# Performance work log

Hardware: AMD Instinct MI355X
Metric: run time of the kernel (lower is better)

## Reference

```python
import jax, jax.numpy as jnp
import numpy as np

DIM = 1024
NHEADS = 16
HEAD_DIM = DIM // NHEADS


def setup_inputs() -> dict:
    key = jax.random.key(0)
    ks = jax.random.split(key, 11)
    B, S = 4, 2048
    scale = 1.0 / np.sqrt(DIM)
    inp = {
        "Q": jax.random.normal(ks[0], (B, S, DIM), jnp.float32),
        "K": jax.random.normal(ks[1], (B, S, DIM), jnp.float32),
        "V": jax.random.normal(ks[2], (B, S, DIM), jnp.float32),
        "Wq": jax.random.normal(ks[3], (DIM, DIM), jnp.float32) * scale,
        "bq": jnp.zeros((DIM,), jnp.float32),
        "Wk": jax.random.normal(ks[4], (DIM, DIM), jnp.float32) * scale,
        "bk": jnp.zeros((DIM,), jnp.float32),
        "Wv": jax.random.normal(ks[5], (DIM, DIM), jnp.float32) * scale,
        "bv": jnp.zeros((DIM,), jnp.float32),
        "Wo": jax.random.normal(ks[6], (DIM, DIM), jnp.float32) * scale,
        "bo": jnp.zeros((DIM,), jnp.float32),
    }
    return inp


def _split_heads(x):
    # [B, S, D] -> [B, H, S, hd]
    B, S, _ = x.shape
    return x.reshape(B, S, NHEADS, HEAD_DIM).transpose(0, 2, 1, 3)


def reference(Q, K, V, Wq, bq, Wk, bk, Wv, bv, Wo, bo):
    q = _split_heads(Q @ Wq + bq)  # [B,H,S,hd]
    k = _split_heads(K @ Wk + bk)
    v = _split_heads(V @ Wv + bv)
    scores = jnp.einsum("bhqd,bhkd->bhqk", q, k) / np.sqrt(HEAD_DIM)
    attn = jax.nn.softmax(scores, axis=-1)  # dropout p=0 -> identity
    out = jnp.einsum("bhqk,bhkd->bhqd", attn, v)  # [B,H,S,hd]
    B, H, S, hd = out.shape
    out = out.transpose(0, 2, 1, 3).reshape(B, S, H * hd)
    return out @ Wo + bo
```

## Files before the change

kernel.cpp:

```cpp
#include <hip/hip_runtime.h>
#include <hip/hip_bf16.h>
#include <math.h>

#define DIM     1024
#define NHEADS  16
#define HD      64
#define BATCH   4
#define SEQ     2048
#define M_TOT   (BATCH * SEQ)
#define QSCALE  0.180336880111f

using short8 = __attribute__((ext_vector_type(8))) short;
using f32x4  = __attribute__((ext_vector_type(4))) float;

__device__ inline unsigned short f2bf(float x) {
    __hip_bfloat16 h = __float2bfloat16(x);
    unsigned short u;
    __builtin_memcpy(&u, &h, sizeof(u));
    return u;
}
__device__ inline void st_o(float* p, float v)          { *p = v; }
__device__ inline void st_o(unsigned short* p, float v) { *p = f2bf(v); }

__device__ inline void async16(const void* g, void* l) {
    __builtin_amdgcn_global_load_lds(
        (const __attribute__((address_space(1))) void*)g,
        (__attribute__((address_space(3))) void*)l, 16, 0, 0);
}

__global__ __launch_bounds__(256) void cvt_bf16(const float* __restrict__ src,
                                                unsigned short* __restrict__ dst) {
    const size_t i = ((size_t)blockIdx.x * 256 + threadIdx.x) * 16;
    unsigned short tmp[16];
    #pragma unroll
    for (int p = 0; p < 4; ++p) {
        const float4 v = *(const float4*)(src + i + p * 4);
        tmp[p * 4 + 0] = f2bf(v.x); tmp[p * 4 + 1] = f2bf(v.y);
        tmp[p * 4 + 2] = f2bf(v.z); tmp[p * 4 + 3] = f2bf(v.w);
    }
    *(short8*)(dst + i)     = *(short8*)&tmp[0];
    *(short8*)(dst + i + 8) = *(short8*)&tmp[8];
}

__global__ __launch_bounds__(256) void wcvt(const float* __restrict__ W,
                                            unsigned short* __restrict__ Wt) {
    __shared__ unsigned short tile[32][33];
    const int t = threadIdx.x;
    const int tx = t & 31, ty = t >> 5;
    const int n0 = blockIdx.x * 32, k0 = blockIdx.y * 32;
    #pragma unroll
    for (int i = 0; i < 4; ++i) {
        const int kk = ty + i * 8;
        tile[kk][tx] = f2bf(W[(size_t)(k0 + kk) * DIM + n0 + tx]);
    }
    __syncthreads();
    #pragma unroll
    for (int i = 0; i < 4; ++i) {
        const int nn = ty + i * 8;
        Wt[(size_t)(n0 + nn) * DIM + k0 + tx] = tile[tx][nn];
    }
}

__global__ __launch_bounds__(256) void vtrans(const unsigned short* __restrict__ vf,
                                              unsigned short* __restrict__ vt) {
    __shared__ unsigned short tile[64][72];
    const int t = threadIdx.x;
    const int b = blockIdx.z, h = blockIdx.y, s0 = blockIdx.x * 64;
    const int r = t >> 2, c = (t & 3) * 16;
    const unsigned short* src = vf + (size_t)(b * SEQ + s0 + r) * DIM + h * HD + c;
    *(short8*)&tile[r][c]     = *(const short8*)src;
    *(short8*)&tile[r][c + 8] = *(const short8*)(src + 8);
    __syncthreads();
    unsigned short tmp[16];
    #pragma unroll
    for (int j = 0; j < 16; ++j) tmp[j] = tile[c + j][r];
    unsigned short* dst = vt + ((size_t)(b * NHEADS + h) * HD + r) * SEQ + s0 + c;
    *(short8*)dst       = *(short8*)&tmp[0];
    *(short8*)(dst + 8) = *(short8*)&tmp[8];
}

template <typename TY>
__global__ __launch_bounds__(256) void gemm_a16(
    const unsigned short* __restrict__ A, const unsigned short* __restrict__ Wt,
    const float* __restrict__ bias, TY* __restrict__ Y, float scale)
{
    __shared__ unsigned short As[128 * 32];
    __shared__ unsigned short Bs[128 * 32];
    const int t = threadIdx.x;
    const int lane = t & 63, wv = t >> 6;
    const int wm = wv >> 1, wn = wv & 1;
    const int l16 = lane & 15, lq = lane >> 4;
    const int m0 = blockIdx.y * 128, n0 = blockIdx.x * 128;
    const int lrow = lane >> 2;
    const int lcol = (lane & 3) * 8;

    f32x4 acc[4][4] = {};

    for (int k0 = 0; k0 < DIM; k0 += 32) {
        #pragma unroll
        for (int c = 0; c < 2; ++c) {
            const int ci  = wv * 2 + c;
            const int row = ci * 16 + lrow;
            async16(A  + (size_t)(m0 + row) * DIM + k0 + lcol, &As[ci * 512]);
            async16(Wt + (size_t)(n0 + row) * DIM + k0 + lcol, &Bs[ci * 512]);
        }
        __syncthreads();

        short8 af[4], bfr[4];
        #pragma unroll
        for (int mi = 0; mi < 4; ++mi)
            af[mi] = *(const short8*)&As[(wm * 64 + mi * 16 + l16) * 32 + lq * 8];
        #pragma unroll
        for (int nj = 0; nj < 4; ++nj)
            bfr[nj] = *(const short8*)&Bs[(wn * 64 + nj * 16 + l16) * 32 + lq * 8];
        #pragma unroll
        for (int mi = 0; mi < 4; ++mi)
            #pragma unroll
            for (int nj = 0; nj < 4; ++nj)
                acc[mi][nj] = __builtin_amdgcn_mfma_f32_16x16x32_bf16(
                    af[mi], bfr[nj], acc[mi][nj], 0, 0, 0);
        __syncthreads();
    }

    #pragma unroll
    for (int mi = 0; mi < 4; ++mi)
        #pragma unroll
        for (int nj = 0; nj < 4; ++nj) {
            const int row = m0 + wm * 64 + mi * 16 + lq * 4;
            const int col = n0 + wn * 64 + nj * 16 + l16;
            const float bb = bias[col];
            #pragma unroll
            for (int r = 0; r < 4; ++r)
                st_o(&Y[(size_t)(row + r) * DIM + col], (acc[mi][nj][r] + bb) * scale);
        }
}

__global__ __launch_bounds__(256) void attn_mfma(
    const unsigned short* qbuf, const unsigned short* __restrict__ kbuf,
    const unsigned short* __restrict__ vtb, unsigned short* ctx)
{
    __shared__ unsigned short Qs[64][72];
    __shared__ unsigned short Ks[64][72];
    __shared__ unsigned short Vs[64][72];
    __shared__ unsigned short Ps[64][72];

    const int t = threadIdx.x;
    const int lane = t & 63, wv = t >> 6;
    const int l16 = lane & 15, lq = lane >> 4;
    const int b = blockIdx.z, h = blockIdx.y;
    const int q0 = blockIdx.x * 64;
    const size_t base  = ((size_t)b * SEQ) * DIM + h * HD;
    const size_t vbase = ((size_t)(b * NHEADS + h)) * HD * SEQ;

    {
        const int r = t >> 2, c = (t & 3) * 16;
        const unsigned short* src = qbuf + base + (size_t)(q0 + r) * DIM + c;
        *(short8*)&Qs[r][c]     = *(const short8*)src;
        *(short8*)&Qs[r][c + 8] = *(const short8*)(src + 8);
    }
    const short8 aq0 = *(const short8*)&Qs[wv * 16 + l16][lq * 8];
    const short8 aq1 = *(const short8*)&Qs[wv * 16 + l16][32 + lq * 8];

    float l_part[4] = {0.f, 0.f, 0.f, 0.f};
    f32x4 O[4] = {};

    for (int s0 = 0; s0 < SEQ; s0 += 64) {
        __syncthreads();
        {
            const int r = t >> 2, c = (t & 3) * 16;
            const unsigned short* src = kbuf + base + (size_t)(s0 + r) * DIM + c;
            *(short8*)&Ks[r][c]     = *(const short8*)src;
            *(short8*)&Ks[r][c + 8] = *(const short8*)(src + 8);
        }
        {
            const int d = t >> 2, c = (t & 3) * 16;
            const unsigned short* src = vtb + vbase + (size_t)d * SEQ + s0 + c;
            *(short8*)&Vs[d][c]     = *(const short8*)src;
            *(short8*)&Vs[d][c + 8] = *(const short8*)(src + 8);
        }
        __syncthreads();

        f32x4 sa[4] = {};
        #pragma unroll
        for (int ti = 0; ti < 4; ++ti) {
            const short8 bk0 = *(const short8*)&Ks[ti * 16 + l16][lq * 8];
            const short8 bk1 = *(const short8*)&Ks[ti * 16 + l16][32 + lq * 8];
            sa[ti] = __builtin_amdgcn_mfma_f32_16x16x32_bf16(aq0, bk0, sa[ti], 0, 0, 0);
            sa[ti] = __builtin_amdgcn_mfma_f32_16x16x32_bf16(aq1, bk1, sa[ti], 0, 0, 0);
        }

        #pragma unroll
        for (int r = 0; r < 4; ++r) {
            const float v0 = __builtin_amdgcn_exp2f(sa[0][r]);
            const float v1 = __builtin_amdgcn_exp2f(sa[1][r]);
            const float v2 = __builtin_amdgcn_exp2f(sa[2][r]);
            const float v3 = __builtin_amdgcn_exp2f(sa[3][r]);
            l_part[r] += (v0 + v1) + (v2 + v3);
            const int prow = wv * 16 + lq * 4 + r;
            Ps[prow][l16]      = f2bf(v0);
            Ps[prow][16 + l16] = f2bf(v1);
            Ps[prow][32 + l16] = f2bf(v2);
            Ps[prow][48 + l16] = f2bf(v3);
        }

        #pragma unroll
        for (int kp = 0; kp < 2; ++kp) {
            const short8 ap = *(const short8*)&Ps[wv * 16 + l16][kp * 32 + lq * 8];
            #pragma unroll
            for (int dt = 0; dt < 4; ++dt) {
                const short8 bv = *(const short8*)&Vs[dt * 16 + l16][kp * 32 + lq * 8];
                O[dt] = __builtin_amdgcn_mfma_f32_16x16x32_bf16(ap, bv, O[dt], 0, 0, 0);
            }
        }
    }

    #pragma unroll
    for (int r = 0; r < 4; ++r) {
        float l = l_part[r];
        #pragma unroll
        for (int msk = 1; msk < 16; msk <<= 1) l += __shfl_xor(l, msk);
        const float inv = 1.0f / l;
        const int orow = wv * 16 + lq * 4 + r;
        #pragma unroll
        for (int dt = 0; dt < 4; ++dt)
            Ps[orow][dt * 16 + l16] = f2bf(O[dt][r] * inv);
    }
    __syncthreads();
    {
        const int r = t >> 2, c = (t & 3) * 16;
        unsigned short* dst = ctx + base + (size_t)(q0 + r) * DIM + c;
        *(short8*)dst       = *(const short8*)&Ps[r][c];
        *(short8*)(dst + 8) = *(const short8*)&Ps[r][c + 8];
    }
}

extern "C" void kernel_launch(void* const* d_in, const int* in_sizes, int n_in,
                              void* d_out, int out_size, void* d_ws, size_t ws_size,
                              hipStream_t stream) {
    const float* Q  = (const float*)d_in[0];
    const float* K  = (const float*)d_in[1];
    const float* V  = (const float*)d_in[2];
    const float* Wq = (const float*)d_in[3];
    const float* bq = (const float*)d_in[4];
    const float* Wk = (const float*)d_in[5];
    const float* bk = (const float*)d_in[6];
    const float* Wv = (const float*)d_in[7];
    const float* bv = (const float*)d_in[8];
    const float* Wo = (const float*)d_in[9];
    const float* bo = (const float*)d_in[10];
    float* out = (float*)d_out;

    const size_t eW = (size_t)DIM * DIM;
    const size_t eB = (size_t)M_TOT * DIM;
    unsigned short* p   = (unsigned short*)d_ws;
    unsigned short* wtq = p; p += eW;
    unsigned short* wtk = p; p += eW;
    unsigned short* wtv = p; p += eW;
    unsigned short* wto = p; p += eW;
    unsigned short* bufA = p; p += eB;
    unsigned short* bufB = p; p += eB;
    unsigned short* bufC = p; p += eB;
    unsigned short* bufD = p; p += eB;
    unsigned short* bufE = p;

    const dim3 gw(32, 32);
    wcvt<<<gw, 256, 0, stream>>>(Wq, wtq);
    wcvt<<<gw, 256, 0, stream>>>(Wk, wtk);
    wcvt<<<gw, 256, 0, stream>>>(Wv, wtv);
    wcvt<<<gw, 256, 0, stream>>>(Wo, wto);

    const int cvt_blocks = (int)(eB / (256 * 16));
    const dim3 gg(DIM / 128, M_TOT / 128);

    cvt_bf16<<<cvt_blocks, 256, 0, stream>>>(V, bufA);
    gemm_a16<unsigned short><<<gg, 256, 0, stream>>>(bufA, wtv, bv, bufC, 1.0f);
    vtrans<<<dim3(SEQ / 64, NHEADS, BATCH), 256, 0, stream>>>(bufC, bufE);

    cvt_bf16<<<cvt_blocks, 256, 0, stream>>>(Q, bufA);
    cvt_bf16<<<cvt_blocks, 256, 0, stream>>>(K, bufB);
    gemm_a16<unsigned short><<<gg, 256, 0, stream>>>(bufA, wtq, bq, bufC, QSCALE);
    gemm_a16<unsigned short><<<gg, 256, 0, stream>>>(bufB, wtk, bk, bufD, 1.0f);

    attn_mfma<<<dim3(SEQ / 64, NHEADS, BATCH), 256, 0, stream>>>(bufC, bufD, bufE, bufC);

    gemm_a16<float><<<gg, 256, 0, stream>>>(bufC, wto, bo, out, 1.0f);
}
```

Baseline: 434.6 us.

## Batch launches, compute V transposed via GEMM, split attention keys across waves

Merges the four weight conversions and the three input conversions into single launches, and fuses the Q and K projections into one grid. It computes V already transposed by swapping GEMM operands with a row bias, which removes the separate transpose kernel. The attention kernel is restructured so each wave handles all 64 queries over its own slice of keys with per-wave LDS and no per-iteration block barriers. Partial outputs and row sums are then reduced across waves through LDS. This cuts launch count and synchronisation, at the cost of more registers per wave and an extra cross-wave reduction at the end.

```diff
diff --git a/kernel.cpp b/kernel.cpp
--- a/kernel.cpp
+++ b/kernel.cpp
@@ -28,22 +28,39 @@
         (__attribute__((address_space(3))) void*)l, 16, 0, 0);
 }
 
-__global__ __launch_bounds__(256) void cvt_bf16(const float* __restrict__ src,
-                                                unsigned short* __restrict__ dst) {
+__global__ __launch_bounds__(256) void cvt3(
+    const float* __restrict__ sq, const float* __restrict__ sk, const float* __restrict__ sv,
+    unsigned short* __restrict__ dq, unsigned short* __restrict__ dk, unsigned short* __restrict__ dv)
+{
+    const float* s; unsigned short* d;
+    if      (blockIdx.y == 0) { s = sq; d = dq; }
+    else if (blockIdx.y == 1) { s = sk; d = dk; }
+    else                      { s = sv; d = dv; }
     const size_t i = ((size_t)blockIdx.x * 256 + threadIdx.x) * 16;
     unsigned short tmp[16];
     #pragma unroll
     for (int p = 0; p < 4; ++p) {
-        const float4 v = *(const float4*)(src + i + p * 4);
-        tmp[p * 4 + 0] = f2bf(v.x); tmp[p * 4 + 1] = f2bf(v.y);
-        tmp[p * 4 + 2] = f2bf(v.z); tmp[p * 4 + 3] = f2bf(v.w);
-    }
-    *(short8*)(dst + i)     = *(short8*)&tmp[0];
-    *(short8*)(dst + i + 8) = *(short8*)&tmp[8];
-}
-
-__global__ __launch_bounds__(256) void wcvt(const float* __restrict__ W,
-                                            unsigned short* __restrict__ Wt) {
+        const float4 v = *(const float4*)(s + i + p * 4);
+        tmp[p*4+0] = f2bf(v.x); tmp[p*4+1] = f2bf(v.y);
+        tmp[p*4+2] = f2bf(v.z); tmp[p*4+3] = f2bf(v.w);
+    }
+    *(short8*)(d + i)     = *(short8*)&tmp[0];
+    *(short8*)(d + i + 8) = *(short8*)&tmp[8];
+}
+
+__global__ __launch_bounds__(256) void wcvt4(
+    const float* __restrict__ w0, const float* __restrict__ w1,
+    const float* __restrict__ w2, const float* __restrict__ w3,
+    unsigned short* __restrict__ o0, unsigned short* __restrict__ o1,
+    unsigned short* __restrict__ o2, unsigned short* __restrict__ o3)
+{
+    const float* W; unsigned short* Wt;
+    switch (blockIdx.z) {
+        case 0:  W = w0; Wt = o0; break;
+        case 1:  W = w1; Wt = o1; break;
+        case 2:  W = w2; Wt = o2; break;
+        default: W = w3; Wt = o3; break;
+    }
     __shared__ unsigned short tile[32][33];
     const int t = threadIdx.x;
     const int tx = t & 31, ty = t >> 5;
@@ -61,28 +78,10 @@
     }
 }
 
-__global__ __launch_bounds__(256) void vtrans(const unsigned short* __restrict__ vf,
-                                              unsigned short* __restrict__ vt) {
-    __shared__ unsigned short tile[64][72];
-    const int t = threadIdx.x;
-    const int b = blockIdx.z, h = blockIdx.y, s0 = blockIdx.x * 64;
-    const int r = t >> 2, c = (t & 3) * 16;
-    const unsigned short* src = vf + (size_t)(b * SEQ + s0 + r) * DIM + h * HD + c;
-    *(short8*)&tile[r][c]     = *(const short8*)src;
-    *(short8*)&tile[r][c + 8] = *(const short8*)(src + 8);
-    __syncthreads();
-    unsigned short tmp[16];
-    #pragma unroll
-    for (int j = 0; j < 16; ++j) tmp[j] = tile[c + j][r];
-    unsigned short* dst = vt + ((size_t)(b * NHEADS + h) * HD + r) * SEQ + s0 + c;
-    *(short8*)dst       = *(short8*)&tmp[0];
-    *(short8*)(dst + 8) = *(short8*)&tmp[8];
-}
-
-template <typename TY>
-__global__ __launch_bounds__(256) void gemm_a16(
-    const unsigned short* __restrict__ A, const unsigned short* __restrict__ Wt,
-    const float* __restrict__ bias, TY* __restrict__ Y, float scale)
+template <bool BROW, typename TY>
+__device__ __forceinline__ void gemm_body(
+    const unsigned short* __restrict__ A, const unsigned short* __restrict__ Bt,
+    const float* __restrict__ bias, TY* __restrict__ Y, int N, float scale)
 {
     __shared__ unsigned short As[128 * 32];
     __shared__ unsigned short Bs[128 * 32];
@@ -91,8 +90,7 @@
     const int wm = wv >> 1, wn = wv & 1;
     const int l16 = lane & 15, lq = lane >> 4;
     const int m0 = blockIdx.y * 128, n0 = blockIdx.x * 128;
-    const int lrow = lane >> 2;
-    const int lcol = (lane & 3) * 8;
+    const int lrow = lane >> 2, lcol = (lane & 3) * 8;
 
     f32x4 acc[4][4] = {};
 
@@ -102,10 +100,9 @@
             const int ci  = wv * 2 + c;
             const int row = ci * 16 + lrow;
             async16(A  + (size_t)(m0 + row) * DIM + k0 + lcol, &As[ci * 512]);
-            async16(Wt + (size_t)(n0 + row) * DIM + k0 + lcol, &Bs[ci * 512]);
+            async16(Bt + (size_t)(n0 + row) * DIM + k0 + lcol, &Bs[ci * 512]);
         }
         __syncthreads();
-
         short8 af[4], bfr[4];
         #pragma unroll
         for (int mi = 0; mi < 4; ++mi)
@@ -128,109 +125,156 @@
         for (int nj = 0; nj < 4; ++nj) {
             const int row = m0 + wm * 64 + mi * 16 + lq * 4;
             const int col = n0 + wn * 64 + nj * 16 + l16;
-            const float bb = bias[col];
-            #pragma unroll
-            for (int r = 0; r < 4; ++r)
-                st_o(&Y[(size_t)(row + r) * DIM + col], (acc[mi][nj][r] + bb) * scale);
-        }
-}
-
+            #pragma unroll
+            for (int r = 0; r < 4; ++r) {
+                const float bb = BROW ? bias[row + r] : bias[col];
+                st_o(&Y[(size_t)(row + r) * N + col], (acc[mi][nj][r] + bb) * scale);
+            }
+        }
+}
+
+__global__ __launch_bounds__(256) void gemm_qk(
+    const unsigned short* Aq, const unsigned short* Wq_, const float* bq_, unsigned short* Yq,
+    const unsigned short* Ak, const unsigned short* Wk_, const float* bk_, unsigned short* Yk)
+{
+    if (blockIdx.z == 0) gemm_body<false>(Aq, Wq_, bq_, Yq, DIM, QSCALE);
+    else                 gemm_body<false>(Ak, Wk_, bk_, Yk, DIM, 1.0f);
+}
+
+__global__ __launch_bounds__(256) void gemm_v(
+    const unsigned short* A, const unsigned short* Bt, const float* bias, unsigned short* Y)
+{
+    gemm_body<true>(A, Bt, bias, Y, M_TOT, 1.0f);
+}
+
+__global__ __launch_bounds__(256) void gemm_out(
+    const unsigned short* A, const unsigned short* Bt, const float* bias, float* Y)
+{
+    gemm_body<false>(A, Bt, bias, Y, DIM, 1.0f);
+}
+
+#define RGN 14848
 __global__ __launch_bounds__(256) void attn_mfma(
     const unsigned short* qbuf, const unsigned short* __restrict__ kbuf,
     const unsigned short* __restrict__ vtb, unsigned short* ctx)
 {
-    __shared__ unsigned short Qs[64][72];
-    __shared__ unsigned short Ks[64][72];
-    __shared__ unsigned short Vs[64][72];
-    __shared__ unsigned short Ps[64][72];
-
-    const int t = threadIdx.x;
-    const int lane = t & 63, wv = t >> 6;
+    __shared__ __align__(16) char smem[4 * RGN];
+    __shared__ float Ls[4][64];
+    const int t = threadIdx.x, lane = t & 63, w = t >> 6;
     const int l16 = lane & 15, lq = lane >> 4;
-    const int b = blockIdx.z, h = blockIdx.y;
-    const int q0 = blockIdx.x * 64;
-    const size_t base  = ((size_t)b * SEQ) * DIM + h * HD;
-    const size_t vbase = ((size_t)(b * NHEADS + h)) * HD * SEQ;
-
-    {
-        const int r = t >> 2, c = (t & 3) * 16;
-        const unsigned short* src = qbuf + base + (size_t)(q0 + r) * DIM + c;
-        *(short8*)&Qs[r][c]     = *(const short8*)src;
-        *(short8*)&Qs[r][c + 8] = *(const short8*)(src + 8);
-    }
-    const short8 aq0 = *(const short8*)&Qs[wv * 16 + l16][lq * 8];
-    const short8 aq1 = *(const short8*)&Qs[wv * 16 + l16][32 + lq * 8];
-
-    float l_part[4] = {0.f, 0.f, 0.f, 0.f};
-    f32x4 O[4] = {};
-
-    for (int s0 = 0; s0 < SEQ; s0 += 64) {
+    const int b = blockIdx.z, h = blockIdx.y, q0 = blockIdx.x * 64;
+    const size_t base = ((size_t)b * SEQ) * DIM + h * HD;
+
+    unsigned short* Kw = (unsigned short*)(smem + w * RGN);
+    unsigned short* Vw = (unsigned short*)(smem + w * RGN + 4608);
+    unsigned short* Pw = (unsigned short*)(smem + w * RGN + 9728);
+
+    short8 aq[4][2];
+    #pragma unroll
+    for (int mi = 0; mi < 4; ++mi)
+        #pragma unroll
+        for (int ks = 0; ks < 2; ++ks)
+            aq[mi][ks] = *(const short8*)(qbuf + base +
+                (size_t)(q0 + mi * 16 + l16) * DIM + ks * 32 + lq * 8);
+
+    float l_part[4][4] = {};
+    f32x4 O[4][4] = {};
+
+    for (int it = 0; it < 16; ++it) {
+        const int s0 = (it * 4 + w) * 32;
+        {
+            const unsigned short* g = kbuf + base + (size_t)(s0 + (lane >> 1)) * DIM + (lane & 1) * 32;
+            unsigned short* d = Kw + (lane >> 1) * 72 + (lane & 1) * 32;
+            #pragma unroll
+            for (int gi = 0; gi < 4; ++gi)
+                *(short8*)(d + gi * 8) = *(const short8*)(g + gi * 8);
+        }
+        {
+            const unsigned short* g = vtb + (size_t)(h * HD + lane) * M_TOT + b * SEQ + s0;
+            unsigned short* d = Vw + lane * 40;
+            #pragma unroll
+            for (int gi = 0; gi < 4; ++gi)
+                *(short8*)(d + gi * 8) = *(const short8*)(g + gi * 8);
+        }
+        f32x4 sc[4][2] = {};
+        #pragma unroll
+        for (int tj = 0; tj < 2; ++tj)
+            #pragma unroll
+            for (int ks = 0; ks < 2; ++ks) {
+                const short8 bk = *(const short8*)(Kw + (tj * 16 + l16) * 72 + ks * 32 + lq * 8);
+                #pragma unroll
+                for (int mi = 0; mi < 4; ++mi)
+                    sc[mi][tj] = __builtin_amdgcn_mfma_f32_16x16x32_bf16(
+                        aq[mi][ks], bk, sc[mi][tj], 0, 0, 0);
+            }
+        #pragma unroll
+        for (int mi = 0; mi < 4; ++mi)
+            #pragma unroll
+            for (int r = 0; r < 4; ++r) {
+                const float v0 = __builtin_amdgcn_exp2f(sc[mi][0][r]);
+                const float v1 = __builtin_amdgcn_exp2f(sc[mi][1][r]);
+                l_part[mi][r] += v0 + v1;
+                const int qr = mi * 16 + lq * 4 + r;
+                Pw[qr * 40 + l16]      = f2bf(v0);
+                Pw[qr * 40 + 16 + l16] = f2bf(v1);
+            }
+        short8 ap[4];
+        #pragma unroll
+        for (int mi = 0; mi < 4; ++mi)
+            ap[mi] = *(const short8*)(Pw + (mi * 16 + l16) * 40 + lq * 8);
+        #pragma unroll
+        for (int dt = 0; dt < 4; ++dt) {
+            const short8 bv = *(const short8*)(Vw + (dt * 16 + l16) * 40 + lq * 8);
+            #pragma unroll
+            for (int mi = 0; mi < 4; ++mi)
+                O[mi][dt] = __builtin_amdgcn_mfma_f32_16x16x32_bf16(
+                    ap[mi], bv, O[mi][dt], 0, 0, 0);
+        }
+    }
+
+    #pragma unroll
+    for (int mi = 0; mi < 4; ++mi)
+        #pragma unroll
+        for (int r = 0; r < 4; ++r) {
+            float l = l_part[mi][r];
+            #pragma unroll
+            for (int msk = 1; msk < 16; msk <<= 1) l += __shfl_xor(l, msk);
+            Ls[w][mi * 16 + lq * 4 + r] = l;
+        }
+
+    #pragma unroll
+    for (int chunk = 0; chunk < 2; ++chunk) {
+        float* Ow = (float*)(smem + w * RGN);
+        #pragma unroll
+        for (int mi = 0; mi < 4; ++mi)
+            #pragma unroll
+            for (int dl = 0; dl < 2; ++dl) {
+                const int dt = chunk * 2 + dl;
+                #pragma unroll
+                for (int r = 0; r < 4; ++r)
+                    Ow[(mi * 16 + lq * 4 + r) * 36 + dl * 16 + l16] = O[mi][dt][r];
+            }
         __syncthreads();
-        {
-            const int r = t >> 2, c = (t & 3) * 16;
-            const unsigned short* src = kbuf + base + (size_t)(s0 + r) * DIM + c;
-            *(short8*)&Ks[r][c]     = *(const short8*)src;
-            *(short8*)&Ks[r][c + 8] = *(const short8*)(src + 8);
-        }
-        {
-            const int d = t >> 2, c = (t & 3) * 16;
-            const unsigned short* src = vtb + vbase + (size_t)d * SEQ + s0 + c;
-            *(short8*)&Vs[d][c]     = *(const short8*)src;
-            *(short8*)&Vs[d][c + 8] = *(const short8*)(src + 8);
-        }
+        const int q  = w * 16 + (lane >> 2);
+        const int ds = (lane & 3) * 8;
+        f32x4 sA = {0.f, 0.f, 0.f, 0.f}, sB = {0.f, 0.f, 0.f, 0.f};
+        float lt = 0.f;
+        #pragma unroll
+        for (int src = 0; src < 4; ++src) {
+            const float* Os = (const float*)(smem + src * RGN);
+            sA += *(const f32x4*)(Os + q * 36 + ds);
+            sB += *(const f32x4*)(Os + q * 36 + ds + 4);
+            lt += Ls[src][q];
+        }
+        const float inv = 1.0f / lt;
+        unsigned short tmp[8];
+        #pragma unroll
+        for (int j = 0; j < 4; ++j) {
+            tmp[j]     = f2bf(sA[j] * inv);
+            tmp[4 + j] = f2bf(sB[j] * inv);
+        }
+        *(short8*)(ctx + base + (size_t)(q0 + q) * DIM + chunk * 32 + ds) = *(short8*)tmp;
         __syncthreads();
-
-        f32x4 sa[4] = {};
-        #pragma unroll
-        for (int ti = 0; ti < 4; ++ti) {
-            const short8 bk0 = *(const short8*)&Ks[ti * 16 + l16][lq * 8];
-            const short8 bk1 = *(const short8*)&Ks[ti * 16 + l16][32 + lq * 8];
-            sa[ti] = __builtin_amdgcn_mfma_f32_16x16x32_bf16(aq0, bk0, sa[ti], 0, 0, 0);
-            sa[ti] = __builtin_amdgcn_mfma_f32_16x16x32_bf16(aq1, bk1, sa[ti], 0, 0, 0);
-        }
-
-        #pragma unroll
-        for (int r = 0; r < 4; ++r) {
-            const float v0 = __builtin_amdgcn_exp2f(sa[0][r]);
-            const float v1 = __builtin_amdgcn_exp2f(sa[1][r]);
-            const float v2 = __builtin_amdgcn_exp2f(sa[2][r]);
-            const float v3 = __builtin_amdgcn_exp2f(sa[3][r]);
-            l_part[r] += (v0 + v1) + (v2 + v3);
-            const int prow = wv * 16 + lq * 4 + r;
-            Ps[prow][l16]      = f2bf(v0);
-            Ps[prow][16 + l16] = f2bf(v1);
-            Ps[prow][32 + l16] = f2bf(v2);
-            Ps[prow][48 + l16] = f2bf(v3);
-        }
-
-        #pragma unroll
-        for (int kp = 0; kp < 2; ++kp) {
-            const short8 ap = *(const short8*)&Ps[wv * 16 + l16][kp * 32 + lq * 8];
-            #pragma unroll
-            for (int dt = 0; dt < 4; ++dt) {
-                const short8 bv = *(const short8*)&Vs[dt * 16 + l16][kp * 32 + lq * 8];
-                O[dt] = __builtin_amdgcn_mfma_f32_16x16x32_bf16(ap, bv, O[dt], 0, 0, 0);
-            }
-        }
-    }
-
-    #pragma unroll
-    for (int r = 0; r < 4; ++r) {
-        float l = l_part[r];
-        #pragma unroll
-        for (int msk = 1; msk < 16; msk <<= 1) l += __shfl_xor(l, msk);
-        const float inv = 1.0f / l;
-        const int orow = wv * 16 + lq * 4 + r;
-        #pragma unroll
-        for (int dt = 0; dt < 4; ++dt)
-            Ps[orow][dt * 16 + l16] = f2bf(O[dt][r] * inv);
-    }
-    __syncthreads();
-    {
-        const int r = t >> 2, c = (t & 3) * 16;
-        unsigned short* dst = ctx + base + (size_t)(q0 + r) * DIM + c;
-        *(short8*)dst       = *(const short8*)&Ps[r][c];
-        *(short8*)(dst + 8) = *(const short8*)&Ps[r][c + 8];
     }
 }
 
@@ -257,31 +301,20 @@
     unsigned short* wtk = p; p += eW;
     unsigned short* wtv = p; p += eW;
     unsigned short* wto = p; p += eW;
-    unsigned short* bufA = p; p += eB;
-    unsigned short* bufB = p; p += eB;
-    unsigned short* bufC = p; p += eB;
-    unsigned short* bufD = p; p += eB;
-    unsigned short* bufE = p;
-
-    const dim3 gw(32, 32);
-    wcvt<<<gw, 256, 0, stream>>>(Wq, wtq);
-    wcvt<<<gw, 256, 0, stream>>>(Wk, wtk);
-    wcvt<<<gw, 256, 0, stream>>>(Wv, wtv);
-    wcvt<<<gw, 256, 0, stream>>>(Wo, wto);
-
-    const int cvt_blocks = (int)(eB / (256 * 16));
-    const dim3 gg(DIM / 128, M_TOT / 128);
-
-    cvt_bf16<<<cvt_blocks, 256, 0, stream>>>(V, bufA);
-    gemm_a16<unsigned short><<<gg, 256, 0, stream>>>(bufA, wtv, bv, bufC, 1.0f);
-    vtrans<<<dim3(SEQ / 64, NHEADS, BATCH), 256, 0, stream>>>(bufC, bufE);
-
-    cvt_bf16<<<cvt_blocks, 256, 0, stream>>>(Q, bufA);
-    cvt_bf16<<<cvt_blocks, 256, 0, stream>>>(K, bufB);
-    gemm_a16<unsigned short><<<gg, 256, 0, stream>>>(bufA, wtq, bq, bufC, QSCALE);
-    gemm_a16<unsigned short><<<gg, 256, 0, stream>>>(bufB, wtk, bk, bufD, 1.0f);
-
-    attn_mfma<<<dim3(SEQ / 64, NHEADS, BATCH), 256, 0, stream>>>(bufC, bufD, bufE, bufC);
-
-    gemm_a16<float><<<gg, 256, 0, stream>>>(bufC, wto, bo, out, 1.0f);
-}
+    unsigned short* X1 = p; p += eB;
+    unsigned short* X2 = p; p += eB;
+    unsigned short* X3 = p; p += eB;
+    unsigned short* X4 = p; p += eB;
+    unsigned short* X5 = p;
+
+    wcvt4<<<dim3(32, 32, 4), 256, 0, stream>>>(Wq, Wk, Wv, Wo, wtq, wtk, wtv, wto);
+    cvt3<<<dim3((unsigned)(eB / (256 * 16)), 3), 256, 0, stream>>>(Q, K, V, X2, X3, X1);
+
+    gemm_v<<<dim3(M_TOT / 128, DIM / 128), 256, 0, stream>>>(wtv, X1, bv, X5);
+    gemm_qk<<<dim3(DIM / 128, M_TOT / 128, 2), 256, 0, stream>>>(
+        X2, wtq, bq, X4,  X3, wtk, bk, X1);
+
+    attn_mfma<<<dim3(SEQ / 64, NHEADS, BATCH), 256, 0, stream>>>(X4, X1, X5, X4);
+
+    gemm_out<<<dim3(DIM / 128, M_TOT / 128), 256, 0, stream>>>(X4, wto, bo, out);
+}
```

After: 458.3 us. 1.05x slower.
